# Performance work log

Hardware: AMD Instinct MI355X
Metric: run time of the kernel (lower is better)

Reference implementation:

```python
import jax, jax.numpy as jnp
import numpy as np

NUM_EXPERTS = 8
HIDDEN = 1024
INTER = 2048
TOKENS = 2048
TOP_K = 2


def setup_inputs() -> dict:
    key = jax.random.key(0)
    k1, k2, k3, k4, k5 = jax.random.split(key, 5)
    hidden_states = jax.random.normal(k1, (TOKENS, HIDDEN), dtype=jnp.float32)
    top_k_index = jax.random.randint(k2, (TOKENS, TOP_K), 0, NUM_EXPERTS, dtype=jnp.int64)
    top_k_weights = jax.random.uniform(k3, (TOKENS, TOP_K), dtype=jnp.float32)
    # parameters, scaled like typical init
    gate_up_proj = jax.random.normal(k4, (NUM_EXPERTS, 2 * INTER, HIDDEN), dtype=jnp.float32) * (HIDDEN ** -0.5)
    down_proj = jax.random.normal(k5, (NUM_EXPERTS, HIDDEN, INTER), dtype=jnp.float32) * (INTER ** -0.5)
    return {
        "hidden_states": hidden_states,
        "top_k_index": top_k_index,
        "top_k_weights": top_k_weights,
        "gate_up_proj": gate_up_proj,
        "down_proj": down_proj,
    }


def reference(hidden_states, top_k_index, top_k_weights, gate_up_proj, down_proj):
    # combine weights per (token, expert): w[t, e] = sum_k 1[idx[t,k]==e] * tw[t,k]
    one_hot = jax.nn.one_hot(top_k_index, NUM_EXPERTS, dtype=hidden_states.dtype)  # [T, K, E]
    combine = jnp.einsum("tke,tk->te", one_hot, top_k_weights)  # [T, E]

    out = jnp.zeros_like(hidden_states)
    # fixed small loop over experts (structural, not a data dim)
    for e in range(NUM_EXPERTS):
        gu = hidden_states @ gate_up_proj[e].T  # [T, 2I]
        gate, up = jnp.split(gu, 2, axis=-1)
        h = jax.nn.gelu(gate, approximate=True) * up  # gelu_pytorch_tanh
        y = h @ down_proj[e].T  # [T, H]
        out = out + y * combine[:, e][:, None]
    return out
```

## Files before the change

kernel.cpp:

```cpp
#include <hip/hip_runtime.h>
#include <stdint.h>

#define T_TOK  2048
#define HID    1024
#define INTERN 2048
#define NEXP   8
#define MAXPOS 5248

typedef __attribute__((ext_vector_type(8))) short          bf16x8;
typedef __attribute__((ext_vector_type(4))) float          f32x4;
typedef __attribute__((ext_vector_type(8))) unsigned short u16x8;
typedef __attribute__((ext_vector_type(4))) unsigned short u16x4;

__device__ __forceinline__ unsigned short f32_to_bf16(float f) {
  unsigned int u = __float_as_uint(f);
  unsigned int r = (u + 0x7FFFu + ((u >> 16) & 1u)) >> 16;
  return (unsigned short)r;
}

__device__ __forceinline__ float bf16_to_f32(unsigned short h) {
  unsigned int u = ((unsigned int)h) << 16;
  return __uint_as_float(u);
}

__device__ __forceinline__ void gload_lds16(const void* g, void* l) {
  __builtin_amdgcn_global_load_lds(
      (const __attribute__((address_space(1))) unsigned int*)g,
      (__attribute__((address_space(3))) unsigned int*)l, 16, 0, 0);
}

__device__ __forceinline__ u16x8 cvt8(float4 a, float4 b) {
  union { u16x8 s; unsigned int u[4]; } r;
  asm("v_cvt_pk_bf16_f32 %0, %1, %2" : "=v"(r.u[0]) : "v"(a.x), "v"(a.y));
  asm("v_cvt_pk_bf16_f32 %0, %1, %2" : "=v"(r.u[1]) : "v"(a.z), "v"(a.w));
  asm("v_cvt_pk_bf16_f32 %0, %1, %2" : "=v"(r.u[2]) : "v"(b.x), "v"(b.y));
  asm("v_cvt_pk_bf16_f32 %0, %1, %2" : "=v"(r.u[3]) : "v"(b.z), "v"(b.w));
  return r.s;
}

#define WAIT_VM0()    asm volatile("s_waitcnt vmcnt(0)" ::: "memory")
#define WAIT_VM4()    asm volatile("s_waitcnt vmcnt(4)" ::: "memory")
#define WAIT_LGKM0()  asm volatile("s_waitcnt lgkmcnt(0)" ::: "memory")
#define SCHED_FENCE() __builtin_amdgcn_sched_barrier(0)

__global__ void route_kernel(const int* __restrict__ tki,
                             const float* __restrict__ tkw,
                             int* __restrict__ counts,
                             int* __restrict__ offsets,
                             int* __restrict__ tok_list,
                             float* __restrict__ w_list,
                             int* __restrict__ pos_map,
                             float* __restrict__ wgt_map) {
  __shared__ int scnt[NEXP];
  __shared__ int soff[NEXP];
  int tid = threadIdx.x;
  if (tid < NEXP) scnt[tid] = 0;
  __syncthreads();
  for (int t = tid; t < T_TOK; t += 256) {
    int e0 = tki[2 * t] & 7;
    int e1 = tki[2 * t + 1] & 7;
    float w0 = tkw[2 * t];
    float w1 = tkw[2 * t + 1];
    if (e0 == e1) {
      int p = atomicAdd(&scnt[e0], 1);
      tok_list[e0 * T_TOK + p] = t;
      w_list [e0 * T_TOK + p] = w0 + w1;
      pos_map[2 * t]     = (p << 3) | e0;
      wgt_map[2 * t]     = w0 + w1;
      pos_map[2 * t + 1] = -1;
      wgt_map[2 * t + 1] = 0.0f;
    } else {
      int p = atomicAdd(&scnt[e0], 1);
      tok_list[e0 * T_TOK + p] = t;
      w_list [e0 * T_TOK + p] = w0;
      pos_map[2 * t]     = (p << 3) | e0;
      wgt_map[2 * t]     = w0;
      int q = atomicAdd(&scnt[e1], 1);
      tok_list[e1 * T_TOK + q] = t;
      w_list [e1 * T_TOK + q] = w1;
      pos_map[2 * t + 1] = (q << 3) | e1;
      wgt_map[2 * t + 1] = w1;
    }
  }
  __syncthreads();
  if (tid == 0) {
    int acc = 0;
    for (int e = 0; e < NEXP; ++e) {
      counts[e]  = scnt[e];
      offsets[e] = acc;
      soff[e]    = acc;
      acc += ((scnt[e] + 127) >> 7) << 7;
    }
  }
  __syncthreads();
  for (int i = tid; i < 2 * T_TOK; i += 256) {
    int v = pos_map[i];
    if (v >= 0) pos_map[i] = soff[v & 7] + (v >> 3);
  }
}

__global__ void gather_cvt_x_kernel(const float* __restrict__ hidden,
                                    const int* __restrict__ counts,
                                    const int* __restrict__ offsets,
                                    const int* __restrict__ tok_list,
                                    unsigned short* __restrict__ xg) {
  int p = blockIdx.x * 2 + (threadIdx.x >> 7);
  int c = threadIdx.x & 127;
  int e = 0;
#pragma unroll
  for (int k = 1; k < NEXP; ++k) if (p >= offsets[k]) e = k;
  int r = p - offsets[e];
  float4 a = {0.f, 0.f, 0.f, 0.f}, b = {0.f, 0.f, 0.f, 0.f};
  if (r < counts[e]) {
    int tok = tok_list[e * T_TOK + r];
    const float4* src = (const float4*)(hidden + (size_t)tok * HID + c * 8);
    a = src[0]; b = src[1];
  }
  *((u16x8*)(xg + (size_t)(p >> 7) * 131072 + c * 1024 + (p & 127) * 8)) = cvt8(a, b);
}

__global__ __launch_bounds__(256, 4)
void gemm1_kernel(const unsigned short* __restrict__ xg,
                  const float* __restrict__ gup,
                  const int* __restrict__ counts,
                  const int* __restrict__ offsets,
                  unsigned short* __restrict__ hbuf) {
  int e  = blockIdx.z;
  int Ne = counts[e];
  int m0 = blockIdx.y * 128;
  if (m0 >= Ne) return;
  int n0  = blockIdx.x * 64;
  int off = offsets[e];

  __shared__ __align__(16) unsigned short As[2][4][128][8];
  __shared__ __align__(16) unsigned short Gs[2][4][64][8];
  __shared__ __align__(16) unsigned short Us[2][4][64][8];

  int tid  = threadIdx.x;
  int lane = tid & 63;
  int wave = tid >> 6;
  int wm = wave >> 1;
  int wn = wave & 1;

  const unsigned short* asrc = xg + (size_t)((off + m0) >> 7) * (HID * 128);

  int brow = tid >> 2;
  int bq   = tid & 3;
  const float* gsrc = gup + (size_t)e * (2 * INTERN) * HID + (size_t)(n0 + brow) * HID + bq * 8;
  const float* usrc = gsrc + (size_t)INTERN * HID;
  int brw = brow ^ bq;

  f32x4 accg[4][2], accu[4][2];
#pragma unroll
  for (int m = 0; m < 4; ++m)
#pragma unroll
    for (int n = 0; n < 2; ++n) {
      accg[m][n] = (f32x4){0.f, 0.f, 0.f, 0.f};
      accu[m][n] = (f32x4){0.f, 0.f, 0.f, 0.f};
    }

  float4 g0, g1, u0, u1;

  {
    char* base = (char*)&As[0][0][0][0];
    gload_lds16(asrc + (size_t)tid * 8,        base + (size_t)tid * 16);
    gload_lds16(asrc + 2048 + (size_t)tid * 8, base + 4096 + (size_t)tid * 16);
    const float4* gp = (const float4*)gsrc;
    const float4* up = (const float4*)usrc;
    float4 tg0 = gp[0], tg1 = gp[1], tu0 = up[0], tu1 = up[1];
    *((u16x8*)&Gs[0][bq][brw][0]) = cvt8(tg0, tg1);
    *((u16x8*)&Us[0][bq][brw][0]) = cvt8(tu0, tu1);
    const float4* gp1 = (const float4*)(gsrc + 32);
    const float4* up1 = (const float4*)(usrc + 32);
    g0 = gp1[0]; g1 = gp1[1]; u0 = up1[0]; u1 = up1[1];
    WAIT_LGKM0(); SCHED_FENCE();
  }

  int cur = 0;
  const int NT = HID / 32;
  for (int t = 0; t < NT; ++t) {
    WAIT_VM4(); SCHED_FENCE();
    __builtin_amdgcn_s_barrier(); SCHED_FENCE();
    int nxt = cur ^ 1;
    int ka = (t + 1 < NT) ? (t + 1) * 32 : 0;
    {
      char* base = (char*)&As[nxt][0][0][0];
      const unsigned short* ak = asrc + (size_t)ka * 128;
      gload_lds16(ak + (size_t)tid * 8,        base + (size_t)tid * 16);
      gload_lds16(ak + 2048 + (size_t)tid * 8, base + 4096 + (size_t)tid * 16);
    }
    SCHED_FENCE();
    {
      int kg = lane >> 4;
      int rl = lane & 15;
      bf16x8 af[4], gf[2], uf[2];
#pragma unroll
      for (int m = 0; m < 4; ++m)
        af[m] = *((const bf16x8*)&As[cur][kg][wm * 64 + m * 16 + rl][0]);
#pragma unroll
      for (int n = 0; n < 2; ++n) {
        int r = (wn * 32 + n * 16 + rl) ^ kg;
        gf[n] = *((const bf16x8*)&Gs[cur][kg][r][0]);
        uf[n] = *((const bf16x8*)&Us[cur][kg][r][0]);
      }
#pragma unroll
      for (int m = 0; m < 4; ++m)
#pragma unroll
        for (int n = 0; n < 2; ++n) {
          accg[m][n] = __builtin_amdgcn_mfma_f32_16x16x32_bf16(af[m], gf[n], accg[m][n], 0, 0, 0);
          accu[m][n] = __builtin_amdgcn_mfma_f32_16x16x32_bf16(af[m], uf[n], accu[m][n], 0, 0, 0);
        }
    }
    *((u16x8*)&Gs[nxt][bq][brw][0]) = cvt8(g0, g1);
    *((u16x8*)&Us[nxt][bq][brw][0]) = cvt8(u0, u1);
    SCHED_FENCE();
    {
      int kb = (t + 2 < NT) ? (t + 2) * 32 : 0;
      const float4* gp = (const float4*)(gsrc + kb);
      const float4* up = (const float4*)(usrc + kb);
      g0 = gp[0]; g1 = gp[1]; u0 = up[0]; u1 = up[1];
    }
    WAIT_LGKM0(); SCHED_FENCE();
    cur = nxt;
  }
  WAIT_VM0();

  int rl = lane & 15;
  int rq = lane >> 4;
  size_t hb_base = (size_t)((off + m0) >> 7) * (INTERN * 128);
#pragma unroll
  for (int m = 0; m < 4; ++m) {
#pragma unroll
    for (int n = 0; n < 2; ++n) {
      int col = n0 + wn * 32 + n * 16 + rl;
      size_t cbase = hb_base + (size_t)(col >> 3) * 1024 + (col & 7);
#pragma unroll
      for (int j = 0; j < 4; ++j) {
        int lr = wm * 64 + m * 16 + rq * 4 + j;
        if (m0 + lr < Ne) {
          float gv = accg[m][n][j];
          float uv = accu[m][n][j];
          float tt2 = gv + 0.044715f * gv * gv * gv;
          float a  = gv / (1.0f + __expf(-1.5957691216f * tt2));
          hbuf[cbase + (size_t)lr * 8] = f32_to_bf16(a * uv);
        }
      }
    }
  }
}

__global__ __launch_bounds__(256, 2)
void gemm2_kernel(const unsigned short* __restrict__ hbuf,
                  const float* __restrict__ down,
                  const int* __restrict__ counts,
                  const int* __restrict__ offsets,
                  unsigned short* __restrict__ ybuf) {
  int e  = blockIdx.z;
  int Ne = counts[e];
  int m0 = blockIdx.y * 128;
  if (m0 >= Ne) return;
  int n0  = blockIdx.x * 64;
  int off = offsets[e];

  __shared__ __align__(16) unsigned short As[2][8][128][8];
  __shared__ __align__(16) unsigned short Bs[2][8][64][8];

  int tid  = threadIdx.x;
  int lane = tid & 63;
  int wave = tid >> 6;
  int wm = wave >> 1;
  int wn = wave & 1;

  const unsigned short* asrc = hbuf + (size_t)((off + m0) >> 7) * (INTERN * 128);

  int brow = tid >> 2;
  int bq   = tid & 3;
  int kgw0 = bq * 2, kgw1 = bq * 2 + 1;
  const float* bsrc = down + (size_t)e * HID * INTERN + (size_t)(n0 + brow) * INTERN + bq * 16;

  f32x4 acc[4][2];
#pragma unroll
  for (int m = 0; m < 4; ++m)
#pragma unroll
    for (int n = 0; n < 2; ++n) acc[m][n] = (f32x4){0.f, 0.f, 0.f, 0.f};

  float4 b0, b1, b2, b3;

  {
    char* base = (char*)&As[0][0][0][0];
#pragma unroll
    for (int o = 0; o < 4; ++o)
      gload_lds16(asrc + o * 2048 + (size_t)tid * 8, base + o * 4096 + (size_t)tid * 16);
    const float4* bp = (const float4*)bsrc;
    float4 t0 = bp[0], t1 = bp[1], t2 = bp[2], t3 = bp[3];
    *((u16x8*)&Bs[0][kgw0][brow ^ kgw0][0]) = cvt8(t0, t1);
    *((u16x8*)&Bs[0][kgw1][brow ^ kgw1][0]) = cvt8(t2, t3);
    const float4* bp1 = (const float4*)(bsrc + 64);
    b0 = bp1[0]; b1 = bp1[1]; b2 = bp1[2]; b3 = bp1[3];
    WAIT_LGKM0(); SCHED_FENCE();
  }

  int cur = 0;
  const int NT = INTERN / 64;
  for (int t = 0; t < NT; ++t) {
    WAIT_VM4(); SCHED_FENCE();
    __builtin_amdgcn_s_barrier(); SCHED_FENCE();
    int nxt = cur ^ 1;
    int ka = (t + 1 < NT) ? (t + 1) * 64 : 0;
    {
      char* base = (char*)&As[nxt][0][0][0];
      const unsigned short* ak = asrc + (size_t)ka * 128;
#pragma unroll
      for (int o = 0; o < 4; ++o)
        gload_lds16(ak + o * 2048 + (size_t)tid * 8, base + o * 4096 + (size_t)tid * 16);
    }
    SCHED_FENCE();
#pragma unroll
    for (int kk = 0; kk < 2; ++kk) {
      int kg = kk * 4 + (lane >> 4);
      int rl = lane & 15;
      bf16x8 af[4], bfv[2];
#pragma unroll
      for (int m = 0; m < 4; ++m)
        af[m] = *((const bf16x8*)&As[cur][kg][wm * 64 + m * 16 + rl][0]);
#pragma unroll
      for (int n = 0; n < 2; ++n)
        bfv[n] = *((const bf16x8*)&Bs[cur][kg][(wn * 32 + n * 16 + rl) ^ kg][0]);
#pragma unroll
      for (int m = 0; m < 4; ++m)
#pragma unroll
        for (int n = 0; n < 2; ++n)
          acc[m][n] = __builtin_amdgcn_mfma_f32_16x16x32_bf16(af[m], bfv[n], acc[m][n], 0, 0, 0);
    }
    *((u16x8*)&Bs[nxt][kgw0][brow ^ kgw0][0]) = cvt8(b0, b1);
    *((u16x8*)&Bs[nxt][kgw1][brow ^ kgw1][0]) = cvt8(b2, b3);
    SCHED_FENCE();
    {
      int kb = (t + 2 < NT) ? (t + 2) * 64 : 0;
      const float4* bp = (const float4*)(bsrc + kb);
      b0 = bp[0]; b1 = bp[1]; b2 = bp[2]; b3 = bp[3];
    }
    WAIT_LGKM0(); SCHED_FENCE();
    cur = nxt;
  }
  WAIT_VM0();

  int rl = lane & 15;
  int rq = lane >> 4;
#pragma unroll
  for (int m = 0; m < 4; ++m) {
#pragma unroll
    for (int n = 0; n < 2; ++n) {
      int col = n0 + wn * 32 + n * 16 + rl;
#pragma unroll
      for (int j = 0; j < 4; ++j) {
        int lr = wm * 64 + m * 16 + rq * 4 + j;
        if (m0 + lr < Ne)
          ybuf[(size_t)(off + m0 + lr) * HID + col] = f32_to_bf16(acc[m][n][j]);
      }
    }
  }
}

__global__ void combine_kernel(const int* __restrict__ pos_map,
                               const float* __restrict__ wgt_map,
                               const unsigned short* __restrict__ ybuf,
                               float* __restrict__ out) {
  int i  = blockIdx.x * 256 + threadIdx.x;
  int t  = i >> 7;
  int c8 = i & 127;
  int p0 = pos_map[2 * t];
  int p1 = pos_map[2 * t + 1];
  float w0 = wgt_map[2 * t];
  float w1 = wgt_map[2 * t + 1];
  float acc[8];
#pragma unroll
  for (int j = 0; j < 8; ++j) acc[j] = 0.f;
  if (p0 >= 0) {
    u16x8 v = *((const u16x8*)(ybuf + (size_t)p0 * HID + c8 * 8));
#pragma unroll
    for (int j = 0; j < 8; ++j) acc[j] += w0 * bf16_to_f32(v[j]);
  }
  if (p1 >= 0) {
    u16x8 v = *((const u16x8*)(ybuf + (size_t)p1 * HID + c8 * 8));
#pragma unroll
    for (int j = 0; j < 8; ++j) acc[j] += w1 * bf16_to_f32(v[j]);
  }
  float4 o0 = make_float4(acc[0], acc[1], acc[2], acc[3]);
  float4 o1 = make_float4(acc[4], acc[5], acc[6], acc[7]);
  float4* dst = (float4*)(out + (size_t)t * HID + c8 * 8);
  dst[0] = o0;
  dst[1] = o1;
}

extern "C" void kernel_launch(void* const* d_in, const int* in_sizes, int n_in,
                              void* d_out, int out_size, void* d_ws, size_t ws_size,
                              hipStream_t stream) {
  (void)in_sizes; (void)n_in; (void)out_size;
  const float* hidden = (const float*)d_in[0];
  const int*   tki    = (const int*)d_in[1];
  const float* tkw    = (const float*)d_in[2];
  const float* gup    = (const float*)d_in[3];
  const float* down   = (const float*)d_in[4];
  float* out = (float*)d_out;
  char*  ws  = (char*)d_ws;

  int*   counts   = (int*)  (ws + 0);
  int*   offsets  = (int*)  (ws + 64);
  int*   tok_list = (int*)  (ws + 256);
  int*   pos_map  = (int*)  (ws + 65792);
  float* wgt_map  = (float*)(ws + 82176);
  float* w_list   = (float*)(ws + 98560);
  unsigned short* hbuf = (unsigned short*)(ws + 4358400);
  unsigned short* ybuf = (unsigned short*)(ws + 25854208);
  unsigned short* xg   = ybuf;

  if (ws_size < 36602112ull) return;

  hipLaunchKernelGGL(route_kernel, dim3(1), dim3(256), 0, stream,
                     tki, tkw, counts, offsets, tok_list, w_list, pos_map, wgt_map);
  hipLaunchKernelGGL(gather_cvt_x_kernel, dim3(MAXPOS / 2), dim3(256), 0, stream,
                     hidden, counts, offsets, tok_list, xg);
  hipLaunchKernelGGL(gemm1_kernel, dim3(INTERN / 64, T_TOK / 128, NEXP), dim3(256), 0, stream,
                     xg, gup, counts, offsets, hbuf);
  hipLaunchKernelGGL(gemm2_kernel, dim3(HID / 64, T_TOK / 128, NEXP), dim3(256), 0, stream,
                     hbuf, down, counts, offsets, ybuf);
  hipLaunchKernelGGL(combine_kernel, dim3(T_TOK * HID / 8 / 256), dim3(256), 0, stream,
                     pos_map, wgt_map, ybuf, out);
}
```

Before: 139.3 us.

## Load gemm1 activation fragments directly from global into registers, bypassing LDS

The activation tile in gemm1 is no longer staged through shared memory with async global-to-LDS copies. Each wave now reads its bf16 A fragments straight from the pre-laid-out xg buffer into registers, one k-step ahead, and ping-pongs between two register sets with the loop unrolled by two. This removes the LDS traffic and the LDS footprint for A. The cost is more registers, reflected in lowering launch bounds from 4 to 3 blocks per CU, and global-load latency now sits directly in each wave's critical path.

```diff
diff --git a/kernel.cpp b/kernel.cpp
--- a/kernel.cpp
+++ b/kernel.cpp
@@ -119,7 +119,52 @@
   *((u16x8*)(xg + (size_t)(p >> 7) * 131072 + c * 1024 + (p & 127) * 8)) = cvt8(a, b);
 }
 
-__global__ __launch_bounds__(256, 4)
+#define G1_STEP(CUR, NXT, T, AFC, AFL)                                                             \
+  {                                                                                                \
+    int kg_ = lane >> 4;                                                                           \
+    int rl_ = lane & 15;                                                                           \
+    bf16x8 gf[2], uf[2];                                                                           \
+    _Pragma("unroll")                                                                              \
+    for (int n = 0; n < 2; ++n) {                                                                  \
+      int r_ = (wn * 32 + n * 16 + rl_) ^ kg_;                                                     \
+      gf[n] = *((const bf16x8*)&Gs[CUR][kg_][r_][0]);                                              \
+      uf[n] = *((const bf16x8*)&Us[CUR][kg_][r_][0]);                                              \
+    }                                                                                              \
+    {                            \
+      int tn_ = ((T) + 1 < NT) ? (T) + 1 : 0;                                                      \
+      const unsigned short* ap_ = afbase + (size_t)(tn_ * 4 + kg_) * 1024 + rl_ * 8 + wm * 512;    \
+      AFL##0 = *((const bf16x8*)(ap_));                                                            \
+      AFL##1 = *((const bf16x8*)(ap_ + 128));                                                      \
+      AFL##2 = *((const bf16x8*)(ap_ + 256));                                                      \
+      AFL##3 = *((const bf16x8*)(ap_ + 384));                                                      \
+    }                                                                                              \
+    SCHED_FENCE();                                                                                 \
+    _Pragma("unroll")                                                                              \
+    for (int n = 0; n < 2; ++n) {                                                                  \
+      accg[0][n] = __builtin_amdgcn_mfma_f32_16x16x32_bf16(AFC##0, gf[n], accg[0][n], 0, 0, 0);    \
+      accu[0][n] = __builtin_amdgcn_mfma_f32_16x16x32_bf16(AFC##0, uf[n], accu[0][n], 0, 0, 0);    \
+      accg[1][n] = __builtin_amdgcn_mfma_f32_16x16x32_bf16(AFC##1, gf[n], accg[1][n], 0, 0, 0);    \
+      accu[1][n] = __builtin_amdgcn_mfma_f32_16x16x32_bf16(AFC##1, uf[n], accu[1][n], 0, 0, 0);    \
+      accg[2][n] = __builtin_amdgcn_mfma_f32_16x16x32_bf16(AFC##2, gf[n], accg[2][n], 0, 0, 0);    \
+      accu[2][n] = __builtin_amdgcn_mfma_f32_16x16x32_bf16(AFC##2, uf[n], accu[2][n], 0, 0, 0);    \
+      accg[3][n] = __builtin_amdgcn_mfma_f32_16x16x32_bf16(AFC##3, gf[n], accg[3][n], 0, 0, 0);    \
+      accu[3][n] = __builtin_amdgcn_mfma_f32_16x16x32_bf16(AFC##3, uf[n], accu[3][n], 0, 0, 0);    \
+    }                                                                                              \
+                                                                     \
+    *((u16x8*)&Gs[NXT][bq][brw][0]) = cvt8(g0, g1);                                                \
+    *((u16x8*)&Us[NXT][bq][brw][0]) = cvt8(u0, u1);                                                \
+    SCHED_FENCE();                                                                                 \
+    {                                                                    \
+      int kb_ = ((T) + 2 < NT) ? ((T) + 2) * 32 : 0;                                               \
+      const float4* gp_ = (const float4*)(gsrc + kb_);                                             \
+      const float4* up_ = (const float4*)(usrc + kb_);                                             \
+      g0 = gp_[0]; g1 = gp_[1]; u0 = up_[0]; u1 = up_[1];                                          \
+    }                                                                                              \
+    WAIT_LGKM0(); SCHED_FENCE();                                                                   \
+    __builtin_amdgcn_s_barrier(); SCHED_FENCE();                                                   \
+  }
+
+__global__ __launch_bounds__(256, 3)
 void gemm1_kernel(const unsigned short* __restrict__ xg,
                   const float* __restrict__ gup,
                   const int* __restrict__ counts,
@@ -132,7 +177,6 @@
   int n0  = blockIdx.x * 64;
   int off = offsets[e];
 
-  __shared__ __align__(16) unsigned short As[2][4][128][8];
   __shared__ __align__(16) unsigned short Gs[2][4][64][8];
   __shared__ __align__(16) unsigned short Us[2][4][64][8];
 
@@ -142,7 +186,7 @@
   int wm = wave >> 1;
   int wn = wave & 1;
 
-  const unsigned short* asrc = xg + (size_t)((off + m0) >> 7) * (HID * 128);
+  const unsigned short* afbase = xg + (size_t)((off + m0) >> 7) * (HID * 128);
 
   int brow = tid >> 2;
   int bq   = tid & 3;
@@ -159,71 +203,36 @@
       accu[m][n] = (f32x4){0.f, 0.f, 0.f, 0.f};
     }
 
+  const int NT = HID / 32;
+
+  bf16x8 afX0, afX1, afX2, afX3;
+  bf16x8 afY0, afY1, afY2, afY3;
   float4 g0, g1, u0, u1;
 
   {
-    char* base = (char*)&As[0][0][0][0];
-    gload_lds16(asrc + (size_t)tid * 8,        base + (size_t)tid * 16);
-    gload_lds16(asrc + 2048 + (size_t)tid * 8, base + 4096 + (size_t)tid * 16);
     const float4* gp = (const float4*)gsrc;
     const float4* up = (const float4*)usrc;
     float4 tg0 = gp[0], tg1 = gp[1], tu0 = up[0], tu1 = up[1];
     *((u16x8*)&Gs[0][bq][brw][0]) = cvt8(tg0, tg1);
     *((u16x8*)&Us[0][bq][brw][0]) = cvt8(tu0, tu1);
+    int kg_ = lane >> 4;
+    int rl_ = lane & 15;
+    const unsigned short* ap = afbase + (size_t)kg_ * 1024 + rl_ * 8 + wm * 512;
+    afX0 = *((const bf16x8*)(ap));
+    afX1 = *((const bf16x8*)(ap + 128));
+    afX2 = *((const bf16x8*)(ap + 256));
+    afX3 = *((const bf16x8*)(ap + 384));
     const float4* gp1 = (const float4*)(gsrc + 32);
     const float4* up1 = (const float4*)(usrc + 32);
     g0 = gp1[0]; g1 = gp1[1]; u0 = up1[0]; u1 = up1[1];
     WAIT_LGKM0(); SCHED_FENCE();
-  }
-
-  int cur = 0;
-  const int NT = HID / 32;
-  for (int t = 0; t < NT; ++t) {
-    WAIT_VM4(); SCHED_FENCE();
     __builtin_amdgcn_s_barrier(); SCHED_FENCE();
-    int nxt = cur ^ 1;
-    int ka = (t + 1 < NT) ? (t + 1) * 32 : 0;
-    {
-      char* base = (char*)&As[nxt][0][0][0];
-      const unsigned short* ak = asrc + (size_t)ka * 128;
-      gload_lds16(ak + (size_t)tid * 8,        base + (size_t)tid * 16);
-      gload_lds16(ak + 2048 + (size_t)tid * 8, base + 4096 + (size_t)tid * 16);
-    }
-    SCHED_FENCE();
-    {
-      int kg = lane >> 4;
-      int rl = lane & 15;
-      bf16x8 af[4], gf[2], uf[2];
-#pragma unroll
-      for (int m = 0; m < 4; ++m)
-        af[m] = *((const bf16x8*)&As[cur][kg][wm * 64 + m * 16 + rl][0]);
-#pragma unroll
-      for (int n = 0; n < 2; ++n) {
-        int r = (wn * 32 + n * 16 + rl) ^ kg;
-        gf[n] = *((const bf16x8*)&Gs[cur][kg][r][0]);
-        uf[n] = *((const bf16x8*)&Us[cur][kg][r][0]);
-      }
-#pragma unroll
-      for (int m = 0; m < 4; ++m)
-#pragma unroll
-        for (int n = 0; n < 2; ++n) {
-          accg[m][n] = __builtin_amdgcn_mfma_f32_16x16x32_bf16(af[m], gf[n], accg[m][n], 0, 0, 0);
-          accu[m][n] = __builtin_amdgcn_mfma_f32_16x16x32_bf16(af[m], uf[n], accu[m][n], 0, 0, 0);
-        }
-    }
-    *((u16x8*)&Gs[nxt][bq][brw][0]) = cvt8(g0, g1);
-    *((u16x8*)&Us[nxt][bq][brw][0]) = cvt8(u0, u1);
-    SCHED_FENCE();
-    {
-      int kb = (t + 2 < NT) ? (t + 2) * 32 : 0;
-      const float4* gp = (const float4*)(gsrc + kb);
-      const float4* up = (const float4*)(usrc + kb);
-      g0 = gp[0]; g1 = gp[1]; u0 = up[0]; u1 = up[1];
-    }
-    WAIT_LGKM0(); SCHED_FENCE();
-    cur = nxt;
-  }
-  WAIT_VM0();
+  }
+
+  for (int tt = 0; tt < NT; tt += 2) {
+    G1_STEP(0, 1, tt,     afX, afY);
+    G1_STEP(1, 0, tt + 1, afY, afX);
+  }
 
   int rl = lane & 15;
   int rq = lane >> 4;
```

New measurement: 142.4 us. 1.02x slower.

## Load A fragments directly to registers and double K-step in gemm1

Applied to the files above, without the earlier changes.

The gemm1 kernel no longer stages the activation tile through LDS; each wave now loads its A fragments straight from global memory into registers, prefetched one step ahead. The K step is doubled from 32 to 64, halving loop iterations and barriers, and the gate/up LDS buffers grow to match. Occupancy bound is lowered from 4 to 3 blocks to leave room for the extra registers. Waves sharing the same rows now load A redundantly from global/L2, and there is no explicit vmcnt wait before using the prefetched registers (the compiler must insert it).

```diff
diff --git a/kernel.cpp b/kernel.cpp
--- a/kernel.cpp
+++ b/kernel.cpp
@@ -119,7 +119,7 @@
   *((u16x8*)(xg + (size_t)(p >> 7) * 131072 + c * 1024 + (p & 127) * 8)) = cvt8(a, b);
 }
 
-__global__ __launch_bounds__(256, 4)
+__global__ __launch_bounds__(256, 3)
 void gemm1_kernel(const unsigned short* __restrict__ xg,
                   const float* __restrict__ gup,
                   const int* __restrict__ counts,
@@ -132,23 +132,26 @@
   int n0  = blockIdx.x * 64;
   int off = offsets[e];
 
-  __shared__ __align__(16) unsigned short As[2][4][128][8];
-  __shared__ __align__(16) unsigned short Gs[2][4][64][8];
-  __shared__ __align__(16) unsigned short Us[2][4][64][8];
+  __shared__ __align__(16) unsigned short Gs[2][8][64][8];
+  __shared__ __align__(16) unsigned short Us[2][8][64][8];
 
   int tid  = threadIdx.x;
   int lane = tid & 63;
   int wave = tid >> 6;
   int wm = wave >> 1;
   int wn = wave & 1;
-
-  const unsigned short* asrc = xg + (size_t)((off + m0) >> 7) * (HID * 128);
+  int kg4 = lane >> 4;
+  int rl  = lane & 15;
+
+  const unsigned short* afbase = xg + (size_t)((off + m0) >> 7) * (HID * 128)
+                               + rl * 8 + wm * 512;
 
   int brow = tid >> 2;
   int bq   = tid & 3;
-  const float* gsrc = gup + (size_t)e * (2 * INTERN) * HID + (size_t)(n0 + brow) * HID + bq * 8;
+  int kgw0 = bq * 2, kgw1 = bq * 2 + 1;
+  int brw0 = brow ^ kgw0, brw1 = brow ^ kgw1;
+  const float* gsrc = gup + (size_t)e * (2 * INTERN) * HID + (size_t)(n0 + brow) * HID + bq * 16;
   const float* usrc = gsrc + (size_t)INTERN * HID;
-  int brw = brow ^ bq;
 
   f32x4 accg[4][2], accu[4][2];
 #pragma unroll
@@ -159,73 +162,104 @@
       accu[m][n] = (f32x4){0.f, 0.f, 0.f, 0.f};
     }
 
-  float4 g0, g1, u0, u1;
+  const int NT = HID / 64;
+
+  bf16x8 a00, a01, a02, a03, a10, a11, a12, a13;
+  float4 g0, g1, g2, g3, u0, u1, u2, u3;
 
   {
-    char* base = (char*)&As[0][0][0][0];
-    gload_lds16(asrc + (size_t)tid * 8,        base + (size_t)tid * 16);
-    gload_lds16(asrc + 2048 + (size_t)tid * 8, base + 4096 + (size_t)tid * 16);
     const float4* gp = (const float4*)gsrc;
     const float4* up = (const float4*)usrc;
-    float4 tg0 = gp[0], tg1 = gp[1], tu0 = up[0], tu1 = up[1];
-    *((u16x8*)&Gs[0][bq][brw][0]) = cvt8(tg0, tg1);
-    *((u16x8*)&Us[0][bq][brw][0]) = cvt8(tu0, tu1);
-    const float4* gp1 = (const float4*)(gsrc + 32);
-    const float4* up1 = (const float4*)(usrc + 32);
-    g0 = gp1[0]; g1 = gp1[1]; u0 = up1[0]; u1 = up1[1];
+    float4 tg0 = gp[0], tg1 = gp[1], tg2 = gp[2], tg3 = gp[3];
+    float4 tu0 = up[0], tu1 = up[1], tu2 = up[2], tu3 = up[3];
+    *((u16x8*)&Gs[0][kgw0][brw0][0]) = cvt8(tg0, tg1);
+    *((u16x8*)&Gs[0][kgw1][brw1][0]) = cvt8(tg2, tg3);
+    *((u16x8*)&Us[0][kgw0][brw0][0]) = cvt8(tu0, tu1);
+    *((u16x8*)&Us[0][kgw1][brw1][0]) = cvt8(tu2, tu3);
+    const unsigned short* ap0 = afbase + (size_t)(0 * 8 + kg4) * 1024;
+    const unsigned short* ap1 = afbase + (size_t)(0 * 8 + 4 + kg4) * 1024;
+    a00 = *((const bf16x8*)(ap0));       a01 = *((const bf16x8*)(ap0 + 128));
+    a02 = *((const bf16x8*)(ap0 + 256)); a03 = *((const bf16x8*)(ap0 + 384));
+    a10 = *((const bf16x8*)(ap1));       a11 = *((const bf16x8*)(ap1 + 128));
+    a12 = *((const bf16x8*)(ap1 + 256)); a13 = *((const bf16x8*)(ap1 + 384));
+    const float4* gp1 = (const float4*)(gsrc + 64);
+    const float4* up1 = (const float4*)(usrc + 64);
+    g0 = gp1[0]; g1 = gp1[1]; g2 = gp1[2]; g3 = gp1[3];
+    u0 = up1[0]; u1 = up1[1]; u2 = up1[2]; u3 = up1[3];
     WAIT_LGKM0(); SCHED_FENCE();
+    __builtin_amdgcn_s_barrier(); SCHED_FENCE();
   }
 
   int cur = 0;
-  const int NT = HID / 32;
   for (int t = 0; t < NT; ++t) {
-    WAIT_VM4(); SCHED_FENCE();
-    __builtin_amdgcn_s_barrier(); SCHED_FENCE();
     int nxt = cur ^ 1;
-    int ka = (t + 1 < NT) ? (t + 1) * 32 : 0;
     {
-      char* base = (char*)&As[nxt][0][0][0];
-      const unsigned short* ak = asrc + (size_t)ka * 128;
-      gload_lds16(ak + (size_t)tid * 8,        base + (size_t)tid * 16);
-      gload_lds16(ak + 2048 + (size_t)tid * 8, base + 4096 + (size_t)tid * 16);
+      bf16x8 gf[2], uf[2];
+      int kg8 = kg4;
+#pragma unroll
+      for (int n = 0; n < 2; ++n) {
+        int r_ = (wn * 32 + n * 16 + rl) ^ kg8;
+        gf[n] = *((const bf16x8*)&Gs[cur][kg8][r_][0]);
+        uf[n] = *((const bf16x8*)&Us[cur][kg8][r_][0]);
+      }
+#pragma unroll
+      for (int n = 0; n < 2; ++n) {
+        accg[0][n] = __builtin_amdgcn_mfma_f32_16x16x32_bf16(a00, gf[n], accg[0][n], 0, 0, 0);
+        accu[0][n] = __builtin_amdgcn_mfma_f32_16x16x32_bf16(a00, uf[n], accu[0][n], 0, 0, 0);
+        accg[1][n] = __builtin_amdgcn_mfma_f32_16x16x32_bf16(a01, gf[n], accg[1][n], 0, 0, 0);
+        accu[1][n] = __builtin_amdgcn_mfma_f32_16x16x32_bf16(a01, uf[n], accu[1][n], 0, 0, 0);
+        accg[2][n] = __builtin_amdgcn_mfma_f32_16x16x32_bf16(a02, gf[n], accg[2][n], 0, 0, 0);
+        accu[2][n] = __builtin_amdgcn_mfma_f32_16x16x32_bf16(a02, uf[n], accu[2][n], 0, 0, 0);
+        accg[3][n] = __builtin_amdgcn_mfma_f32_16x16x32_bf16(a03, gf[n], accg[3][n], 0, 0, 0);
+        accu[3][n] = __builtin_amdgcn_mfma_f32_16x16x32_bf16(a03, uf[n], accu[3][n], 0, 0, 0);
+      }
+      kg8 = 4 + kg4;
+#pragma unroll
+      for (int n = 0; n < 2; ++n) {
+        int r_ = (wn * 32 + n * 16 + rl) ^ kg8;
+        gf[n] = *((const bf16x8*)&Gs[cur][kg8][r_][0]);
+        uf[n] = *((const bf16x8*)&Us[cur][kg8][r_][0]);
+      }
+#pragma unroll
+      for (int n = 0; n < 2; ++n) {
+        accg[0][n] = __builtin_amdgcn_mfma_f32_16x16x32_bf16(a10, gf[n], accg[0][n], 0, 0, 0);
+        accu[0][n] = __builtin_amdgcn_mfma_f32_16x16x32_bf16(a10, uf[n], accu[0][n], 0, 0, 0);
+        accg[1][n] = __builtin_amdgcn_mfma_f32_16x16x32_bf16(a11, gf[n], accg[1][n], 0, 0, 0);
+        accu[1][n] = __builtin_amdgcn_mfma_f32_16x16x32_bf16(a11, uf[n], accu[1][n], 0, 0, 0);
+        accg[2][n] = __builtin_amdgcn_mfma_f32_16x16x32_bf16(a12, gf[n], accg[2][n], 0, 0, 0);
+        accu[2][n] = __builtin_amdgcn_mfma_f32_16x16x32_bf16(a12, uf[n], accu[2][n], 0, 0, 0);
+        accg[3][n] = __builtin_amdgcn_mfma_f32_16x16x32_bf16(a13, gf[n], accg[3][n], 0, 0, 0);
+        accu[3][n] = __builtin_amdgcn_mfma_f32_16x16x32_bf16(a13, uf[n], accu[3][n], 0, 0, 0);
+      }
     }
     SCHED_FENCE();
     {
-      int kg = lane >> 4;
-      int rl = lane & 15;
-      bf16x8 af[4], gf[2], uf[2];
-#pragma unroll
-      for (int m = 0; m < 4; ++m)
-        af[m] = *((const bf16x8*)&As[cur][kg][wm * 64 + m * 16 + rl][0]);
-#pragma unroll
-      for (int n = 0; n < 2; ++n) {
-        int r = (wn * 32 + n * 16 + rl) ^ kg;
-        gf[n] = *((const bf16x8*)&Gs[cur][kg][r][0]);
-        uf[n] = *((const bf16x8*)&Us[cur][kg][r][0]);
-      }
-#pragma unroll
-      for (int m = 0; m < 4; ++m)
-#pragma unroll
-        for (int n = 0; n < 2; ++n) {
-          accg[m][n] = __builtin_amdgcn_mfma_f32_16x16x32_bf16(af[m], gf[n], accg[m][n], 0, 0, 0);
-          accu[m][n] = __builtin_amdgcn_mfma_f32_16x16x32_bf16(af[m], uf[n], accu[m][n], 0, 0, 0);
-        }
-    }
-    *((u16x8*)&Gs[nxt][bq][brw][0]) = cvt8(g0, g1);
-    *((u16x8*)&Us[nxt][bq][brw][0]) = cvt8(u0, u1);
+      int tn = (t + 1 < NT) ? t + 1 : 0;
+      const unsigned short* ap0 = afbase + (size_t)(tn * 8 + kg4) * 1024;
+      const unsigned short* ap1 = afbase + (size_t)(tn * 8 + 4 + kg4) * 1024;
+      a00 = *((const bf16x8*)(ap0));       a01 = *((const bf16x8*)(ap0 + 128));
+      a02 = *((const bf16x8*)(ap0 + 256)); a03 = *((const bf16x8*)(ap0 + 384));
+      a10 = *((const bf16x8*)(ap1));       a11 = *((const bf16x8*)(ap1 + 128));
+      a12 = *((const bf16x8*)(ap1 + 256)); a13 = *((const bf16x8*)(ap1 + 384));
+    }
+    SCHED_FENCE();
+    *((u16x8*)&Gs[nxt][kgw0][brw0][0]) = cvt8(g0, g1);
+    *((u16x8*)&Gs[nxt][kgw1][brw1][0]) = cvt8(g2, g3);
+    *((u16x8*)&Us[nxt][kgw0][brw0][0]) = cvt8(u0, u1);
+    *((u16x8*)&Us[nxt][kgw1][brw1][0]) = cvt8(u2, u3);
     SCHED_FENCE();
     {
-      int kb = (t + 2 < NT) ? (t + 2) * 32 : 0;
+      int kb = (t + 2 < NT) ? (t + 2) * 64 : 0;
       const float4* gp = (const float4*)(gsrc + kb);
       const float4* up = (const float4*)(usrc + kb);
-      g0 = gp[0]; g1 = gp[1]; u0 = up[0]; u1 = up[1];
+      g0 = gp[0]; g1 = gp[1]; g2 = gp[2]; g3 = gp[3];
+      u0 = up[0]; u1 = up[1]; u2 = up[2]; u3 = up[3];
     }
     WAIT_LGKM0(); SCHED_FENCE();
+    __builtin_amdgcn_s_barrier(); SCHED_FENCE();
     cur = nxt;
   }
-  WAIT_VM0();
-
-  int rl = lane & 15;
+
   int rq = lane >> 4;
   size_t hb_base = (size_t)((off + m0) >> 7) * (INTERN * 128);
 #pragma unroll
```

New measurement: 142.2 us. +2.1%, slower.

## Stage fp32 gate/up weights to LDS via direct loads, read activations from registers

Applied to the files above, without the earlier changes.

gemm1 now copies raw fp32 gate/up weight tiles straight into LDS with global_load_lds and converts them to bf16 while building the MFMA fragments, instead of converting them in registers before the LDS store. Activation fragments are no longer staged through LDS. Each wave loads its A fragments directly from global memory into registers, prefetching the next k-step between MFMA groups. This removes the A-tile LDS traffic and the register-side weight conversion path. In exchange it doubles the LDS footprint for the weights, adds a full vmcnt(0) wait plus barrier every iteration, and duplicates A global loads across the waves that share the same rows.

```diff
diff --git a/kernel.cpp b/kernel.cpp
--- a/kernel.cpp
+++ b/kernel.cpp
@@ -36,6 +36,12 @@
   asm("v_cvt_pk_bf16_f32 %0, %1, %2" : "=v"(r.u[2]) : "v"(b.x), "v"(b.y));
   asm("v_cvt_pk_bf16_f32 %0, %1, %2" : "=v"(r.u[3]) : "v"(b.z), "v"(b.w));
   return r.s;
+}
+
+__device__ __forceinline__ bf16x8 cvt8b(float4 a, float4 b) {
+  union { u16x8 s; bf16x8 b; } r2;
+  r2.s = cvt8(a, b);
+  return r2.b;
 }
 
 #define WAIT_VM0()    asm volatile("s_waitcnt vmcnt(0)" ::: "memory")
@@ -132,23 +138,24 @@
   int n0  = blockIdx.x * 64;
   int off = offsets[e];
 
-  __shared__ __align__(16) unsigned short As[2][4][128][8];
-  __shared__ __align__(16) unsigned short Gs[2][4][64][8];
-  __shared__ __align__(16) unsigned short Us[2][4][64][8];
+  __shared__ __align__(16) float Gf[2][2][4][64][4];
+  __shared__ __align__(16) float Uf[2][2][4][64][4];
 
   int tid  = threadIdx.x;
   int lane = tid & 63;
   int wave = tid >> 6;
   int wm = wave >> 1;
   int wn = wave & 1;
-
-  const unsigned short* asrc = xg + (size_t)((off + m0) >> 7) * (HID * 128);
-
-  int brow = tid >> 2;
-  int bq   = tid & 3;
-  const float* gsrc = gup + (size_t)e * (2 * INTERN) * HID + (size_t)(n0 + brow) * HID + bq * 8;
-  const float* usrc = gsrc + (size_t)INTERN * HID;
-  int brw = brow ^ bq;
+  int kg4 = lane >> 4;
+  int rl  = lane & 15;
+
+  const unsigned short* afbase = xg + (size_t)((off + m0) >> 7) * (HID * 128)
+                               + rl * 8 + wm * 512;
+
+  int brow = tid & 63;
+  int bfq  = tid >> 6;
+  const float* gsrcD = gup + (size_t)e * (2 * INTERN) * HID + (size_t)(n0 + brow) * HID + bfq * 4;
+  const float* usrcD = gsrcD + (size_t)INTERN * HID;
 
   f32x4 accg[4][2], accu[4][2];
 #pragma unroll
@@ -159,73 +166,85 @@
       accu[m][n] = (f32x4){0.f, 0.f, 0.f, 0.f};
     }
 
-  float4 g0, g1, u0, u1;
+  const int NT = HID / 32;
+
+  bf16x8 af0, af1, af2, af3;
 
   {
-    char* base = (char*)&As[0][0][0][0];
-    gload_lds16(asrc + (size_t)tid * 8,        base + (size_t)tid * 16);
-    gload_lds16(asrc + 2048 + (size_t)tid * 8, base + 4096 + (size_t)tid * 16);
-    const float4* gp = (const float4*)gsrc;
-    const float4* up = (const float4*)usrc;
-    float4 tg0 = gp[0], tg1 = gp[1], tu0 = up[0], tu1 = up[1];
-    *((u16x8*)&Gs[0][bq][brw][0]) = cvt8(tg0, tg1);
-    *((u16x8*)&Us[0][bq][brw][0]) = cvt8(tu0, tu1);
-    const float4* gp1 = (const float4*)(gsrc + 32);
-    const float4* up1 = (const float4*)(usrc + 32);
-    g0 = gp1[0]; g1 = gp1[1]; u0 = up1[0]; u1 = up1[1];
-    WAIT_LGKM0(); SCHED_FENCE();
+    char* gb = (char*)&Gf[0][0][0][0][0];
+    char* ub = (char*)&Uf[0][0][0][0][0];
+    gload_lds16(gsrcD,      gb + (size_t)tid * 16);
+    gload_lds16(gsrcD + 16, gb + 4096 + (size_t)tid * 16);
+    gload_lds16(usrcD,      ub + (size_t)tid * 16);
+    gload_lds16(usrcD + 16, ub + 4096 + (size_t)tid * 16);
+    const unsigned short* ap = afbase + (size_t)kg4 * 1024;
+    af0 = *((const bf16x8*)(ap));
+    af1 = *((const bf16x8*)(ap + 128));
+    af2 = *((const bf16x8*)(ap + 256));
+    af3 = *((const bf16x8*)(ap + 384));
+    WAIT_VM0(); SCHED_FENCE();
+    __builtin_amdgcn_s_barrier(); SCHED_FENCE();
   }
 
   int cur = 0;
-  const int NT = HID / 32;
   for (int t = 0; t < NT; ++t) {
-    WAIT_VM4(); SCHED_FENCE();
-    __builtin_amdgcn_s_barrier(); SCHED_FENCE();
     int nxt = cur ^ 1;
-    int ka = (t + 1 < NT) ? (t + 1) * 32 : 0;
     {
-      char* base = (char*)&As[nxt][0][0][0];
-      const unsigned short* ak = asrc + (size_t)ka * 128;
-      gload_lds16(ak + (size_t)tid * 8,        base + (size_t)tid * 16);
-      gload_lds16(ak + 2048 + (size_t)tid * 8, base + 4096 + (size_t)tid * 16);
+      int kb = (t + 1 < NT) ? (t + 1) * 32 : 0;
+      char* gb = (char*)&Gf[nxt][0][0][0][0];
+      char* ub = (char*)&Uf[nxt][0][0][0][0];
+      gload_lds16(gsrcD + kb,      gb + (size_t)tid * 16);
+      gload_lds16(gsrcD + kb + 16, gb + 4096 + (size_t)tid * 16);
+      gload_lds16(usrcD + kb,      ub + (size_t)tid * 16);
+      gload_lds16(usrcD + kb + 16, ub + 4096 + (size_t)tid * 16);
     }
     SCHED_FENCE();
     {
-      int kg = lane >> 4;
-      int rl = lane & 15;
-      bf16x8 af[4], gf[2], uf[2];
-#pragma unroll
-      for (int m = 0; m < 4; ++m)
-        af[m] = *((const bf16x8*)&As[cur][kg][wm * 64 + m * 16 + rl][0]);
+      int half = kg4 >> 1;
+      int fq0  = (kg4 & 1) * 2;
+      bf16x8 gf[2], uf[2];
 #pragma unroll
       for (int n = 0; n < 2; ++n) {
-        int r = (wn * 32 + n * 16 + rl) ^ kg;
-        gf[n] = *((const bf16x8*)&Gs[cur][kg][r][0]);
-        uf[n] = *((const bf16x8*)&Us[cur][kg][r][0]);
-      }
-#pragma unroll
-      for (int m = 0; m < 4; ++m)
-#pragma unroll
-        for (int n = 0; n < 2; ++n) {
-          accg[m][n] = __builtin_amdgcn_mfma_f32_16x16x32_bf16(af[m], gf[n], accg[m][n], 0, 0, 0);
-          accu[m][n] = __builtin_amdgcn_mfma_f32_16x16x32_bf16(af[m], uf[n], accu[m][n], 0, 0, 0);
-        }
-    }
-    *((u16x8*)&Gs[nxt][bq][brw][0]) = cvt8(g0, g1);
-    *((u16x8*)&Us[nxt][bq][brw][0]) = cvt8(u0, u1);
-    SCHED_FENCE();
-    {
-      int kb = (t + 2 < NT) ? (t + 2) * 32 : 0;
-      const float4* gp = (const float4*)(gsrc + kb);
-      const float4* up = (const float4*)(usrc + kb);
-      g0 = gp[0]; g1 = gp[1]; u0 = up[0]; u1 = up[1];
-    }
-    WAIT_LGKM0(); SCHED_FENCE();
+        int r_ = wn * 32 + n * 16 + rl;
+        float4 ga = *((const float4*)&Gf[cur][half][fq0][r_][0]);
+        float4 gb2 = *((const float4*)&Gf[cur][half][fq0 + 1][r_][0]);
+        float4 ua = *((const float4*)&Uf[cur][half][fq0][r_][0]);
+        float4 ub2 = *((const float4*)&Uf[cur][half][fq0 + 1][r_][0]);
+        gf[n] = cvt8b(ga, gb2);
+        uf[n] = cvt8b(ua, ub2);
+      }
+      int tn = (t + 1 < NT) ? t + 1 : 0;
+      const unsigned short* apn = afbase + (size_t)(tn * 4 + kg4) * 1024;
+#pragma unroll
+      for (int n = 0; n < 2; ++n) {
+        accg[0][n] = __builtin_amdgcn_mfma_f32_16x16x32_bf16(af0, gf[n], accg[0][n], 0, 0, 0);
+        accu[0][n] = __builtin_amdgcn_mfma_f32_16x16x32_bf16(af0, uf[n], accu[0][n], 0, 0, 0);
+      }
+      af0 = *((const bf16x8*)(apn));
+#pragma unroll
+      for (int n = 0; n < 2; ++n) {
+        accg[1][n] = __builtin_amdgcn_mfma_f32_16x16x32_bf16(af1, gf[n], accg[1][n], 0, 0, 0);
+        accu[1][n] = __builtin_amdgcn_mfma_f32_16x16x32_bf16(af1, uf[n], accu[1][n], 0, 0, 0);
+      }
+      af1 = *((const bf16x8*)(apn + 128));
+#pragma unroll
+      for (int n = 0; n < 2; ++n) {
+        accg[2][n] = __builtin_amdgcn_mfma_f32_16x16x32_bf16(af2, gf[n], accg[2][n], 0, 0, 0);
+        accu[2][n] = __builtin_amdgcn_mfma_f32_16x16x32_bf16(af2, uf[n], accu[2][n], 0, 0, 0);
+      }
+      af2 = *((const bf16x8*)(apn + 256));
+#pragma unroll
+      for (int n = 0; n < 2; ++n) {
+        accg[3][n] = __builtin_amdgcn_mfma_f32_16x16x32_bf16(af3, gf[n], accg[3][n], 0, 0, 0);
+        accu[3][n] = __builtin_amdgcn_mfma_f32_16x16x32_bf16(af3, uf[n], accu[3][n], 0, 0, 0);
+      }
+      af3 = *((const bf16x8*)(apn + 384));
+    }
+    WAIT_VM0(); SCHED_FENCE();
+    __builtin_amdgcn_s_barrier(); SCHED_FENCE();
     cur = nxt;
   }
-  WAIT_VM0();
-
-  int rl = lane & 15;
+
   int rq = lane >> 4;
   size_t hb_base = (size_t)((off + m0) >> 7) * (INTERN * 128);
 #pragma unroll
```

New measurement: 173.4 us. 1.24x slower.
